# Kernel optimization log

Measured on AMD Instinct MI355X. Metric: run time of the kernel, lower is better.

Reference implementation:

```python
import jax, jax.numpy as jnp
import numpy as np

CHANNEL_N = 16
RESET_PROB = 0.5
ALIVE_THRESH = 0.1


def _perceive_kernel(c):
    # Faithful reproduction of the TF kernel construction:
    # stack([sobel_x, sobel_y, identity], axis=0) -> (3,3,3); expand_dims(-2);
    # repeat over channels -> (3,3,C,3). Depthwise conv treats axis0 as filter
    # height and the last axis as the channel multiplier (same as tf code).
    sx = jnp.array([[-1.0, 0.0, 1.0], [-2.0, 0.0, 2.0], [-1.0, 0.0, 1.0]], jnp.float32) / 8.0
    sy = sx.T
    ident = jnp.zeros((3, 3), jnp.float32).at[1, 1].set(1.0)
    k = jnp.stack([sx, sy, ident], axis=0)          # (3,3,3)
    k = jnp.repeat(k[:, :, None, :], c, axis=2)     # (3,3,C,3)
    # TF depthwise output ordering: out_ch = c*multiplier + m -> flatten (C,3)
    return k.reshape(3, 3, 1, c * 3)                # HWIO for grouped conv


def _alive_mask(x):
    # 3x3 max-pool (stride 1, SAME) on alpha channel, thresholded.
    alpha = x[..., 3:4]
    pooled = jax.lax.reduce_window(alpha, -jnp.inf, jax.lax.max,
                                   (1, 3, 3, 1), (1, 1, 1, 1), 'SAME')
    return pooled > ALIVE_THRESH


def setup_inputs() -> dict:
    key = jax.random.key(0)
    k1, k2, k3, k4, k5, k6 = jax.random.split(key, 6)
    B, H, W, C = 32, 256, 256, CHANNEL_N
    x = jax.random.uniform(k1, (B, H, W, C), dtype=jnp.float32)
    rand_mask = jax.random.uniform(k2, (B, H, W, 1), dtype=jnp.float32)
    W1 = jax.random.normal(k3, (3 * C, 128), dtype=jnp.float32) * 0.1
    b1 = jax.random.normal(k4, (128,), dtype=jnp.float32) * 0.1
    W2 = jax.random.normal(k5, (128, C), dtype=jnp.float32) * 0.1
    b2 = jax.random.normal(k6, (C,), dtype=jnp.float32) * 0.1
    return {"x": x, "rand_mask": rand_mask, "W1": W1, "b1": b1, "W2": W2, "b2": b2}


def reference(x, rand_mask, W1, b1, W2, b2):
    C = x.shape[-1]
    pre_update_mask = _alive_mask(x)
    # perceive: depthwise stencil conv, multiplier 3 -> (N,H,W,3C)
    kern = _perceive_kernel(C)
    y = jax.lax.conv_general_dilated(
        x, kern, window_strides=(1, 1), padding='SAME',
        dimension_numbers=('NHWC', 'HWIO', 'NHWC'), feature_group_count=C)
    # rule model: per-cell 1x1 MLP
    h = jax.nn.relu(jnp.einsum('nhwk,kd->nhwd', y, W1) + b1)
    dx = jnp.einsum('nhwd,dc->nhwc', h, W2) + b2
    # stochastic update mask
    upd = (rand_mask < RESET_PROB).astype(x.dtype)
    x = x + dx * upd
    post_update_mask = _alive_mask(x)
    life_mask = jnp.logical_and(pre_update_mask, post_update_mask).astype(x.dtype)
    return x * life_mask
```

## Files before the change

### kernel.cpp

```cpp
#include <hip/hip_runtime.h>

typedef __bf16 bf16x8 __attribute__((ext_vector_type(8)));
typedef float f32x4 __attribute__((ext_vector_type(4)));

#define XS_COLS 130
#define XS_CHP_B 32
#define XS_SLOT_B (XS_COLS * XS_CHP_B)
#define H_BYTES 16384
#define OFF_XS H_BYTES
#define SMEM_BYTES (H_BYTES + 4 * XS_SLOT_B)

__device__ __forceinline__ unsigned short bfbits(float f) {
    __bf16 b = (__bf16)f;
    return __builtin_bit_cast(unsigned short, b);
}

__global__ __launch_bounds__(512, 4) void nca_main(
    const float* __restrict__ x, const float* __restrict__ rm,
    const float* __restrict__ W1, const float* __restrict__ b1,
    const float* __restrict__ W2, const float* __restrict__ b2,
    float* __restrict__ out, unsigned int* __restrict__ am)
{
    __shared__ __align__(16) char smem[SMEM_BYTES];
    char* Hb  = smem;
    char* XSb = smem + OFF_XS;

    const int tid  = threadIdx.x;
    const int lane = tid & 63;
    const int wid  = tid >> 6;
    const int lrow = lane & 15;
    const int kg   = lane >> 4;
    const int kgh  = kg >> 1;
    const int kgl  = kg & 1;

    int raw = blockIdx.x;
    int wg  = (raw & 7) * 256 + (raw >> 3);
    int img = wg >> 6;
    int rem = wg & 63;
    int w0  = (rem >> 5) << 7;
    int h0  = (rem & 31) * 8;

    const size_t imgbase = (size_t)img * 65536;

    const int r  = wid >> 1;
    const int cq = wid & 1;

    bf16x8 wt[2][3];
    #pragma unroll
    for (int m = 0; m < 2; ++m) {
        int n = (r * 2 + m) * 16 + lrow;
        #pragma unroll
        for (int kk = 0; kk < 3; ++kk) {
            float c0, c1, c2;
            if (kk == 0) {
                c0 = kgh ? -0.25f : -0.125f; c1 = 0.f; c2 = kgh ? 0.25f : 0.125f;
            } else if (kk == 1) {
                c0 = kgh ? -0.125f : -0.125f;
                c1 = kgh ? -0.25f  : 0.f;
                c2 = kgh ? -0.125f : 0.125f;
            } else {
                c0 = kgh ? 0.f : 0.125f; c1 = kgh ? 1.f : 0.25f; c2 = kgh ? 0.f : 0.125f;
            }
            bf16x8 v;
            #pragma unroll
            for (int j = 0; j < 8; ++j) {
                int ch = kgl * 8 + j;
                float wv = c0 * W1[(3 * ch + 0) * 128 + n]
                         + c1 * W1[(3 * ch + 1) * 128 + n]
                         + c2 * W1[(3 * ch + 2) * 128 + n];
                v[j] = (__bf16)wv;
            }
            wt[m][kk] = v;
        }
    }

    bf16x8 w2f[4];
    #pragma unroll
    for (int kk = 0; kk < 4; ++kk) {
        bf16x8 v;
        #pragma unroll
        for (int j = 0; j < 8; ++j) {
            int k = kk * 32 + kg * 8 + j;
            v[j] = (__bf16)W2[k * 16 + lrow];
        }
        w2f[kk] = v;
    }

    f32x4 b1q[2];
    #pragma unroll
    for (int m = 0; m < 2; ++m)
        b1q[m] = *reinterpret_cast<const f32x4*>(b1 + (r * 2 + m) * 16 + kg * 4);
    const f32x4 b2q = *reinterpret_cast<const f32x4*>(b2 + kg * 4);

    auto g1 = [&](int half, int sbm, int sb0, int sbp) {
        #pragma unroll
        for (int t = 0; t < 2; ++t) {
            int pxl = cq * 32 + t * 16 + lrow;
            int pxg = half * 64 + pxl;
            int colbase = (pxg + 1) * XS_CHP_B + kgl * 16;
            const char* a0p = XSb + sbm + colbase + (kgh ? 0 : -XS_CHP_B);
            const char* a1p = kgh ? (XSb + sb0 + colbase - XS_CHP_B) : (XSb + sbm + colbase + XS_CHP_B);
            const char* a2p = kgh ? (XSb + sbp + colbase)            : (XSb + sb0 + colbase + XS_CHP_B);
            bf16x8 bf0 = *reinterpret_cast<const bf16x8*>(a0p);
            bf16x8 bf1 = *reinterpret_cast<const bf16x8*>(a1p);
            bf16x8 bf2 = *reinterpret_cast<const bf16x8*>(a2p);
            f32x4 a0 = {0.f, 0.f, 0.f, 0.f}, a1 = {0.f, 0.f, 0.f, 0.f};
            a0 = __builtin_amdgcn_mfma_f32_16x16x32_bf16(wt[0][0], bf0, a0, 0, 0, 0);
            a1 = __builtin_amdgcn_mfma_f32_16x16x32_bf16(wt[1][0], bf0, a1, 0, 0, 0);
            a0 = __builtin_amdgcn_mfma_f32_16x16x32_bf16(wt[0][1], bf1, a0, 0, 0, 0);
            a1 = __builtin_amdgcn_mfma_f32_16x16x32_bf16(wt[1][1], bf1, a1, 0, 0, 0);
            a0 = __builtin_amdgcn_mfma_f32_16x16x32_bf16(wt[0][2], bf2, a0, 0, 0, 0);
            a1 = __builtin_amdgcn_mfma_f32_16x16x32_bf16(wt[1][2], bf2, a1, 0, 0, 0);
            #pragma unroll
            for (int m = 0; m < 2; ++m) {
                f32x4 hv = m ? a1 : a0;
                f32x4 bq = b1q[m];
                ushort4 q;
                q.x = bfbits(fmaxf(hv[0] + bq[0], 0.f));
                q.y = bfbits(fmaxf(hv[1] + bq[1], 0.f));
                q.z = bfbits(fmaxf(hv[2] + bq[2], 0.f));
                q.w = bfbits(fmaxf(hv[3] + bq[3], 0.f));
                int n0 = (r * 2 + m) * 16 + kg * 4;
                int chunk = (n0 >> 3) ^ (pxl & 7);
                *reinterpret_cast<ushort4*>(Hb + pxl * 256 + chunk * 16 + ((n0 >> 2) & 1) * 8) = q;
            }
        }
    };

    auto g2epi = [&](int half, int w4, int h) {
        int pxl2 = w4 * 16 + lrow;
        f32x4 acc2 = {0.f, 0.f, 0.f, 0.f};
        #pragma unroll
        for (int kk = 0; kk < 4; ++kk) {
            int chunk = (4 * kk + kg) ^ (pxl2 & 7);
            bf16x8 hb = *reinterpret_cast<const bf16x8*>(Hb + pxl2 * 256 + chunk * 16);
            acc2 = __builtin_amdgcn_mfma_f32_16x16x32_bf16(w2f[kk], hb, acc2, 0, 0, 0);
        }
        size_t pix = imgbase + (size_t)h * 256 + w0 + half * 64 + pxl2;
        float upd = (rm[pix] < 0.5f) ? 1.f : 0.f;
        float4 xv = *reinterpret_cast<const float4*>(x + pix * 16 + kg * 4);
        float4 xn;
        xn.x = xv.x + (acc2[0] + b2q[0]) * upd;
        xn.y = xv.y + (acc2[1] + b2q[1]) * upd;
        xn.z = xv.z + (acc2[2] + b2q[2]) * upd;
        xn.w = xv.w + (acc2[3] + b2q[3]) * upd;
        *reinterpret_cast<float4*>(out + pix * 16 + kg * 4) = xn;
        if (kg == 0) {
            unsigned int av = ((unsigned int)bfbits(xv.w) << 16) | (unsigned int)bfbits(xn.w);
            am[pix] = av;
        }
    };

    auto stage = [&](int gh2) {
        int slot = (gh2 + 4) & 3;
        int tid2 = tid - 256;
        #pragma unroll
        for (int k = 0; k < 3; ++k) {
            int idx = tid2 + k * 256;
            if (idx < 520) {
                int col = idx >> 2, chq = idx & 3;
                int gw = w0 + col - 1;
                float4 v = make_float4(0.f, 0.f, 0.f, 0.f);
                if (gh2 < 256 && gw >= 0 && gw < 256)
                    v = *reinterpret_cast<const float4*>(x + (imgbase + (size_t)gh2 * 256 + gw) * 16 + chq * 4);
                ushort4 q = { bfbits(v.x), bfbits(v.y), bfbits(v.z), bfbits(v.w) };
                *reinterpret_cast<ushort4*>(XSb + slot * XS_SLOT_B + col * XS_CHP_B + chq * 8) = q;
            }
        }
    };

    #pragma unroll
    for (int rr = 0; rr < 3; ++rr) {
        int gh = h0 - 1 + rr;
        int slot = (gh + 4) & 3;
        for (int idx = tid; idx < 520; idx += 512) {
            int col = idx >> 2, chq = idx & 3;
            int gw = w0 + col - 1;
            float4 v = make_float4(0.f, 0.f, 0.f, 0.f);
            if (gh >= 0 && gh < 256 && gw >= 0 && gw < 256)
                v = *reinterpret_cast<const float4*>(x + (imgbase + (size_t)gh * 256 + gw) * 16 + chq * 4);
            ushort4 q = { bfbits(v.x), bfbits(v.y), bfbits(v.z), bfbits(v.w) };
            *reinterpret_cast<ushort4*>(XSb + slot * XS_SLOT_B + col * XS_CHP_B + chq * 8) = q;
        }
    }
    __syncthreads();

    for (int i = 0; i < 8; ++i) {
        int h = h0 + i;
        int sbm = ((h + 3) & 3) * XS_SLOT_B;
        int sb0 = ((h + 4) & 3) * XS_SLOT_B;
        int sbp = ((h + 5) & 3) * XS_SLOT_B;

        g1(0, sbm, sb0, sbp);
        __syncthreads();

        if (wid < 4)      g2epi(0, wid, h);
        else if (i < 7)   stage(h + 2);
        __syncthreads();

        g1(1, sbm, sb0, sbp);
        __syncthreads();

        if (wid >= 4)     g2epi(1, wid - 4, h);
        __syncthreads();
    }
}

__global__ __launch_bounds__(256) void nca_life(
    const unsigned int* __restrict__ am, float* __restrict__ out)
{
    int q = blockIdx.x * 256 + threadIdx.x;
    int w = q & 255, hh = (q >> 8) & 255;
    float mn = -1e30f, mo = -1e30f;
    #pragma unroll
    for (int dh = -1; dh <= 1; ++dh) {
        int h2 = hh + dh;
        if (h2 < 0 || h2 > 255) continue;
        #pragma unroll
        for (int dw = -1; dw <= 1; ++dw) {
            int w2 = w + dw;
            if (w2 < 0 || w2 > 255) continue;
            unsigned int v = am[q + dh * 256 + dw];
            mn = fmaxf(mn, __uint_as_float(v << 16));
            mo = fmaxf(mo, __uint_as_float(v & 0xffff0000u));
        }
    }
    if (!(mo > 0.1f && mn > 0.1f)) {
        float4 z = make_float4(0.f, 0.f, 0.f, 0.f);
        float4* o = (float4*)(out + (size_t)q * 16);
        o[0] = z; o[1] = z; o[2] = z; o[3] = z;
    }
}

extern "C" void kernel_launch(void* const* d_in, const int* in_sizes, int n_in,
                              void* d_out, int out_size, void* d_ws, size_t ws_size,
                              hipStream_t stream) {
    (void)in_sizes; (void)n_in; (void)out_size; (void)ws_size;
    const float* x  = (const float*)d_in[0];
    const float* rm = (const float*)d_in[1];
    const float* W1 = (const float*)d_in[2];
    const float* b1 = (const float*)d_in[3];
    const float* W2 = (const float*)d_in[4];
    const float* b2 = (const float*)d_in[5];
    float* out = (float*)d_out;
    unsigned int* am = (unsigned int*)d_ws;

    nca_main<<<dim3(2048), dim3(512), 0, stream>>>(x, rm, W1, b1, W2, b2, out, am);
    nca_life<<<dim3(8192), dim3(256), 0, stream>>>(am, out);
}
```

Before: 138.5 us.

## Halve tile width to 64 columns and double the workgroup count

Each workgroup now covers a 64-wide by 8-row strip instead of 128 wide, and the launch doubles to 4096 blocks. The two-half g1/g2 sequence becomes a single pass per row, cutting barriers per row from four to two, and the staging buffer shrinks. In exchange the halo fraction grows (66 of 64 columns are loaded), there are more blocks, and fewer waves do useful MFMA work per barrier phase.

```diff
diff --git a/kernel.cpp b/kernel.cpp
--- a/kernel.cpp
+++ b/kernel.cpp
@@ -3,7 +3,7 @@
 typedef __bf16 bf16x8 __attribute__((ext_vector_type(8)));
 typedef float f32x4 __attribute__((ext_vector_type(4)));
 
-#define XS_COLS 130
+#define XS_COLS 66
 #define XS_CHP_B 32
 #define XS_SLOT_B (XS_COLS * XS_CHP_B)
 #define H_BYTES 16384
@@ -34,11 +34,11 @@
     const int kgl  = kg & 1;
 
     int raw = blockIdx.x;
-    int wg  = (raw & 7) * 256 + (raw >> 3);
-    int img = wg >> 6;
-    int rem = wg & 63;
-    int w0  = (rem >> 5) << 7;
-    int h0  = (rem & 31) * 8;
+    int wg  = (raw & 7) * 512 + (raw >> 3);
+    int img = wg >> 7;
+    int rem = wg & 127;
+    int h0  = (rem >> 2) * 8;
+    int w0  = (rem & 3) << 6;
 
     const size_t imgbase = (size_t)img * 65536;
 
@@ -92,12 +92,30 @@
         b1q[m] = *reinterpret_cast<const f32x4*>(b1 + (r * 2 + m) * 16 + kg * 4);
     const f32x4 b2q = *reinterpret_cast<const f32x4*>(b2 + kg * 4);
 
-    auto g1 = [&](int half, int sbm, int sb0, int sbp) {
+    for (int idx = tid; idx < 3 * 264; idx += 512) {
+        int rr  = idx / 264;
+        int q   = idx - rr * 264;
+        int col = q >> 2, chq = q & 3;
+        int gh = h0 - 1 + rr, gw = w0 + col - 1;
+        int slot = (gh + 4) & 3;
+        float4 v = make_float4(0.f, 0.f, 0.f, 0.f);
+        if (gh >= 0 && gh < 256 && gw >= 0 && gw < 256)
+            v = *reinterpret_cast<const float4*>(x + (imgbase + (size_t)gh * 256 + gw) * 16 + chq * 4);
+        ushort4 qq = { bfbits(v.x), bfbits(v.y), bfbits(v.z), bfbits(v.w) };
+        *reinterpret_cast<ushort4*>(XSb + slot * XS_SLOT_B + col * XS_CHP_B + chq * 8) = qq;
+    }
+    __syncthreads();
+
+    for (int i = 0; i < 8; ++i) {
+        int h = h0 + i;
+        int sbm = ((h + 3) & 3) * XS_SLOT_B;
+        int sb0 = ((h + 4) & 3) * XS_SLOT_B;
+        int sbp = ((h + 5) & 3) * XS_SLOT_B;
+
         #pragma unroll
         for (int t = 0; t < 2; ++t) {
             int pxl = cq * 32 + t * 16 + lrow;
-            int pxg = half * 64 + pxl;
-            int colbase = (pxg + 1) * XS_CHP_B + kgl * 16;
+            int colbase = (pxl + 1) * XS_CHP_B + kgl * 16;
             const char* a0p = XSb + sbm + colbase + (kgh ? 0 : -XS_CHP_B);
             const char* a1p = kgh ? (XSb + sb0 + colbase - XS_CHP_B) : (XSb + sbm + colbase + XS_CHP_B);
             const char* a2p = kgh ? (XSb + sbp + colbase)            : (XSb + sb0 + colbase + XS_CHP_B);
@@ -125,83 +143,48 @@
                 *reinterpret_cast<ushort4*>(Hb + pxl * 256 + chunk * 16 + ((n0 >> 2) & 1) * 8) = q;
             }
         }
-    };
-
-    auto g2epi = [&](int half, int w4, int h) {
-        int pxl2 = w4 * 16 + lrow;
-        f32x4 acc2 = {0.f, 0.f, 0.f, 0.f};
-        #pragma unroll
-        for (int kk = 0; kk < 4; ++kk) {
-            int chunk = (4 * kk + kg) ^ (pxl2 & 7);
-            bf16x8 hb = *reinterpret_cast<const bf16x8*>(Hb + pxl2 * 256 + chunk * 16);
-            acc2 = __builtin_amdgcn_mfma_f32_16x16x32_bf16(w2f[kk], hb, acc2, 0, 0, 0);
-        }
-        size_t pix = imgbase + (size_t)h * 256 + w0 + half * 64 + pxl2;
-        float upd = (rm[pix] < 0.5f) ? 1.f : 0.f;
-        float4 xv = *reinterpret_cast<const float4*>(x + pix * 16 + kg * 4);
-        float4 xn;
-        xn.x = xv.x + (acc2[0] + b2q[0]) * upd;
-        xn.y = xv.y + (acc2[1] + b2q[1]) * upd;
-        xn.z = xv.z + (acc2[2] + b2q[2]) * upd;
-        xn.w = xv.w + (acc2[3] + b2q[3]) * upd;
-        *reinterpret_cast<float4*>(out + pix * 16 + kg * 4) = xn;
-        if (kg == 0) {
-            unsigned int av = ((unsigned int)bfbits(xv.w) << 16) | (unsigned int)bfbits(xn.w);
-            am[pix] = av;
-        }
-    };
-
-    auto stage = [&](int gh2) {
-        int slot = (gh2 + 4) & 3;
-        int tid2 = tid - 256;
-        #pragma unroll
-        for (int k = 0; k < 3; ++k) {
-            int idx = tid2 + k * 256;
-            if (idx < 520) {
-                int col = idx >> 2, chq = idx & 3;
-                int gw = w0 + col - 1;
-                float4 v = make_float4(0.f, 0.f, 0.f, 0.f);
-                if (gh2 < 256 && gw >= 0 && gw < 256)
-                    v = *reinterpret_cast<const float4*>(x + (imgbase + (size_t)gh2 * 256 + gw) * 16 + chq * 4);
-                ushort4 q = { bfbits(v.x), bfbits(v.y), bfbits(v.z), bfbits(v.w) };
-                *reinterpret_cast<ushort4*>(XSb + slot * XS_SLOT_B + col * XS_CHP_B + chq * 8) = q;
-            }
-        }
-    };
-
-    #pragma unroll
-    for (int rr = 0; rr < 3; ++rr) {
-        int gh = h0 - 1 + rr;
-        int slot = (gh + 4) & 3;
-        for (int idx = tid; idx < 520; idx += 512) {
-            int col = idx >> 2, chq = idx & 3;
-            int gw = w0 + col - 1;
-            float4 v = make_float4(0.f, 0.f, 0.f, 0.f);
-            if (gh >= 0 && gh < 256 && gw >= 0 && gw < 256)
-                v = *reinterpret_cast<const float4*>(x + (imgbase + (size_t)gh * 256 + gw) * 16 + chq * 4);
-            ushort4 q = { bfbits(v.x), bfbits(v.y), bfbits(v.z), bfbits(v.w) };
-            *reinterpret_cast<ushort4*>(XSb + slot * XS_SLOT_B + col * XS_CHP_B + chq * 8) = q;
-        }
-    }
-    __syncthreads();
-
-    for (int i = 0; i < 8; ++i) {
-        int h = h0 + i;
-        int sbm = ((h + 3) & 3) * XS_SLOT_B;
-        int sb0 = ((h + 4) & 3) * XS_SLOT_B;
-        int sbp = ((h + 5) & 3) * XS_SLOT_B;
-
-        g1(0, sbm, sb0, sbp);
         __syncthreads();
 
-        if (wid < 4)      g2epi(0, wid, h);
-        else if (i < 7)   stage(h + 2);
-        __syncthreads();
-
-        g1(1, sbm, sb0, sbp);
-        __syncthreads();
-
-        if (wid >= 4)     g2epi(1, wid - 4, h);
+        if (wid < 4) {
+            const int pxl2 = wid * 16 + lrow;
+            f32x4 acc2 = {0.f, 0.f, 0.f, 0.f};
+            #pragma unroll
+            for (int kk = 0; kk < 4; ++kk) {
+                int chunk = (4 * kk + kg) ^ (pxl2 & 7);
+                bf16x8 hb = *reinterpret_cast<const bf16x8*>(Hb + pxl2 * 256 + chunk * 16);
+                acc2 = __builtin_amdgcn_mfma_f32_16x16x32_bf16(w2f[kk], hb, acc2, 0, 0, 0);
+            }
+            size_t pix = imgbase + (size_t)h * 256 + w0 + pxl2;
+            float upd = (rm[pix] < 0.5f) ? 1.f : 0.f;
+            float4 xv = *reinterpret_cast<const float4*>(x + pix * 16 + kg * 4);
+            float4 xn;
+            xn.x = xv.x + (acc2[0] + b2q[0]) * upd;
+            xn.y = xv.y + (acc2[1] + b2q[1]) * upd;
+            xn.z = xv.z + (acc2[2] + b2q[2]) * upd;
+            xn.w = xv.w + (acc2[3] + b2q[3]) * upd;
+            *reinterpret_cast<float4*>(out + pix * 16 + kg * 4) = xn;
+            if (kg == 0) {
+                unsigned int av = ((unsigned int)bfbits(xv.w) << 16) | (unsigned int)bfbits(xn.w);
+                am[pix] = av;
+            }
+        } else if (i < 7) {
+            const int gh2 = h + 2;
+            int slot = (gh2 + 4) & 3;
+            int tid2 = tid - 256;
+            #pragma unroll
+            for (int k = 0; k < 2; ++k) {
+                int idx = tid2 + k * 256;
+                if (idx < 264) {
+                    int col = idx >> 2, chq = idx & 3;
+                    int gw = w0 + col - 1;
+                    float4 v = make_float4(0.f, 0.f, 0.f, 0.f);
+                    if (gh2 < 256 && gw >= 0 && gw < 256)
+                        v = *reinterpret_cast<const float4*>(x + (imgbase + (size_t)gh2 * 256 + gw) * 16 + chq * 4);
+                    ushort4 q = { bfbits(v.x), bfbits(v.y), bfbits(v.z), bfbits(v.w) };
+                    *reinterpret_cast<ushort4*>(XSb + slot * XS_SLOT_B + col * XS_CHP_B + chq * 8) = q;
+                }
+            }
+        }
         __syncthreads();
     }
 }
@@ -245,6 +228,6 @@
     float* out = (float*)d_out;
     unsigned int* am = (unsigned int*)d_ws;
 
-    nca_main<<<dim3(2048), dim3(512), 0, stream>>>(x, rm, W1, b1, W2, b2, out, am);
+    nca_main<<<dim3(4096), dim3(512), 0, stream>>>(x, rm, W1, b1, W2, b2, out, am);
     nca_life<<<dim3(8192), dim3(256), 0, stream>>>(am, out);
 }
```

After: 153.2 us. +10.7%, slower.
